# Kernel tuning notes

Measured on AMD Instinct MI355X. Metric: run time of the kernel, lower is better.

The kernel has to match this reference:

```python
import jax, jax.numpy as jnp
import numpy as np

EPSILON = 0.1


def setup_inputs() -> dict:
    key = jax.random.key(0)
    ks = jax.random.split(key, 6)
    N, E, F_IN, F_OUT, NF = 50000, 800000, 256, 96, 3
    x = jax.random.normal(ks[0], (N, F_IN), dtype=jnp.float32)
    adj_vals = jax.random.uniform(ks[1], (E,), dtype=jnp.float32)
    d_scales = jax.random.uniform(ks[2], (NF, N), dtype=jnp.float32)
    # xavier-uniform-ish weights
    limit = np.sqrt(6.0 / (F_IN + F_OUT)).astype(np.float32)
    weights = jax.random.uniform(ks[3], (NF, F_IN, F_OUT), dtype=jnp.float32,
                                 minval=-limit, maxval=limit)
    bias = jnp.zeros((F_OUT,), dtype=jnp.float32)
    edge_index = jax.random.randint(ks[4], (2, E), 0, N, dtype=jnp.int32)
    return {"x": x, "adj_vals": adj_vals, "d_scales": d_scales,
            "weights": weights, "bias": bias, "edge_index": edge_index}


def reference(x, adj_vals, d_scales, weights, bias, edge_index):
    N = x.shape[0]
    row, col = edge_index[0], edge_index[1]

    # degree with self loops (add_remaining_self_loops adds 1 per node)
    deg = jax.ops.segment_sum(jnp.ones_like(adj_vals), row, num_segments=N) + 1.0
    eps_deg_inv = EPSILON / deg  # [N], diagonal of sparse_degree(..., epsilon)

    def spmm(t):  # symadj @ t via edge list
        return jax.ops.segment_sum(adj_vals[:, None] * t[col], row, num_segments=N)

    out = jnp.zeros((N, weights.shape[2]), dtype=x.dtype)
    n_filters = weights.shape[0]
    for ii in range(n_filters):
        sign = -1.0 if ii == 0 else 1.0  # Ad = symadj -/+ eps*diag(deg^-1)
        t = d_scales[ii][:, None] * (x @ weights[ii])          # D @ (x W)
        t = spmm(t) + sign * eps_deg_inv[:, None] * t          # Ad @ t
        t = d_scales[ii][:, None] * jax.nn.relu(t)             # D @ relu(t)
        out = out + t
    return out + bias
```

## Files before the change

kernel.cpp:

```cpp
#include <hip/hip_runtime.h>

#define EPSILON 0.1f
#define F_IN 256
#define F_OUT 96
#define NF 3
#define TCOLS 288
#define TSTRIDE 320
#define CAP 64
#define BN 96
#define CW 104
#define NCVT (TCOLS * F_IN / 4)

#define RPB 64
#define NBINS 782
#define BCAP 1536
#define EPB 2048
#define GPAD 32

typedef __attribute__((ext_vector_type(8))) short bf8_t;
typedef __attribute__((ext_vector_type(4))) float f32x4;

__device__ inline ushort f2b(float f) {
    union { float f; unsigned u; } v; v.f = f;
    unsigned u = v.u;
    return (ushort)((u + 0x7FFFu + ((u >> 16) & 1u)) >> 16);
}
__device__ inline float blo(unsigned u) { return __uint_as_float(u << 16); }
__device__ inline float bhi(unsigned u) { return __uint_as_float(u & 0xffff0000u); }

__device__ inline bf8_t cvt8(float4 a, float4 b) {
    bf8_t r;
    r[0] = (short)f2b(a.x); r[1] = (short)f2b(a.y);
    r[2] = (short)f2b(a.z); r[3] = (short)f2b(a.w);
    r[4] = (short)f2b(b.x); r[5] = (short)f2b(b.y);
    r[6] = (short)f2b(b.z); r[7] = (short)f2b(b.w);
    return r;
}

__global__ __launch_bounds__(256) void setup_kernel(const float* __restrict__ w,
                                                    ushort* __restrict__ wt,
                                                    int* __restrict__ gcur) {
    int tid = blockIdx.x * 256 + threadIdx.x;
    if (tid < NCVT) {
        int base = tid * 4;
        int gc = base >> 8;
        int k  = base & 255;
        int ii = gc / F_OUT;
        int c  = gc - ii * F_OUT;
        const float* wp = w + (size_t)ii * (F_IN * F_OUT) + (size_t)k * F_OUT + c;
        ushort4 o;
        o.x = f2b(wp[0 * F_OUT]);
        o.y = f2b(wp[1 * F_OUT]);
        o.z = f2b(wp[2 * F_OUT]);
        o.w = f2b(wp[3 * F_OUT]);
        *(ushort4*)(wt + base) = o;
    } else {
        int z = (tid - NCVT) * 4;
        if (z + 3 < NBINS * GPAD) {
            *(int4*)(gcur + z) = make_int4(0, 0, 0, 0);
        }
    }
}

__global__ __launch_bounds__(256) void bin_cvt_kernel(
        const int* __restrict__ row, const int* __restrict__ col,
        const float* __restrict__ vals, int E,
        int* __restrict__ gcur, int2* __restrict__ gout,
        const float* __restrict__ x, ushort* __restrict__ xb, int N, int nbin) {
    __shared__ int hist[NBINS];
    __shared__ int gbase[NBINS];

    if ((int)blockIdx.x < nbin) {
        int tid = threadIdx.x;
        for (int i = tid; i < NBINS; i += 256) hist[i] = 0;
        __syncthreads();

        int e0 = (int)blockIdx.x * EPB;
        int4 r4[2], c4[2]; float4 v4[2];
        int rank[8], binv[8], valv[8];
        unsigned recx[8];
        #pragma unroll
        for (int g = 0; g < 2; ++g) {
            int e = e0 + tid * 4 + g * 1024;
            if (e + 3 < E) {
                r4[g] = *(const int4*)(row + e);
                c4[g] = *(const int4*)(col + e);
                v4[g] = *(const float4*)(vals + e);
            } else {
                int4 rr, cc; float4 vv;
                int* rp = (int*)&rr; int* cp = (int*)&cc; float* vp = (float*)&vv;
                #pragma unroll
                for (int j = 0; j < 4; ++j) {
                    int ee = e + j;
                    rp[j] = (ee < E) ? row[ee] : -1;
                    cp[j] = (ee < E) ? col[ee] : 0;
                    vp[j] = (ee < E) ? vals[ee] : 0.f;
                }
                r4[g] = rr; c4[g] = cc; v4[g] = vv;
            }
        }
        #pragma unroll
        for (int g = 0; g < 2; ++g) {
            const int* rp = (const int*)&r4[g];
            const int* cp = (const int*)&c4[g];
            const float* vp = (const float*)&v4[g];
            #pragma unroll
            for (int j = 0; j < 4; ++j) {
                int s = g * 4 + j;
                int r = rp[j];
                if (r >= 0) {
                    int b = r >> 6;
                    binv[s] = b;
                    recx[s] = (unsigned)(cp[j] & 0xffff) |
                              ((unsigned)(r & 63) << 16) | ((unsigned)b << 22);
                    valv[s] = __float_as_int(vp[j]);
                    rank[s] = atomicAdd(&hist[b], 1);
                } else {
                    binv[s] = -1; rank[s] = 0; recx[s] = 0; valv[s] = 0;
                }
            }
        }
        __syncthreads();

        #pragma unroll
        for (int q = 0; q < 4; ++q) {
            int i = threadIdx.x * 4 + q;
            if (i < NBINS) {
                int h = hist[i];
                gbase[i] = h ? atomicAdd(&gcur[i * GPAD], h) : 0;
            }
        }
        __syncthreads();

        #pragma unroll
        for (int s = 0; s < 8; ++s) {
            int b = binv[s];
            if (b >= 0) {
                int pos = gbase[b] + rank[s];
                if (pos < BCAP)
                    gout[(size_t)b * BCAP + pos] = make_int2((int)recx[s], valv[s]);
            }
        }
    } else {
        size_t base = ((size_t)((int)blockIdx.x - nbin) * 256 + threadIdx.x) * 8;
        if (base < (size_t)N * F_IN) {
            float4 a = *(const float4*)(x + base);
            float4 b = *(const float4*)(x + base + 4);
            bf8_t o = cvt8(a, b);
            *(bf8_t*)(xb + base) = o;
        }
    }
}

__global__ __launch_bounds__(512) void gemm_bucket(
        const ushort* __restrict__ xb, const ushort* __restrict__ wt,
        const float* __restrict__ dsc, ushort* __restrict__ t, int N,
        int nper, int nw,
        const int2* __restrict__ gout, const int* __restrict__ gcur,
        int* __restrict__ cnt, int2* __restrict__ evs2) {
    __shared__ ushort Bs[BN * F_IN];

    int tid = threadIdx.x;

    if ((int)blockIdx.x < NBINS) {
        int2* buck = (int2*)Bs;
        int*  lcnt = (int*)(Bs + 16384);
        int b = blockIdx.x;
        if (tid < RPB) lcnt[tid] = 0;
        __syncthreads();

        int nrec = gcur[b * GPAD];
        if (nrec > BCAP) nrec = BCAP;
        for (int i = tid; i < nrec; i += 512) {
            int2 rec = gout[(size_t)b * BCAP + i];
            int rl = (rec.x >> 16) & 63;
            int c  = rec.x & 0xffff;
            int k = atomicAdd(&lcnt[rl], 1);
            if (k < CAP) buck[rl * CAP + k] = make_int2(c * TSTRIDE, rec.y);
        }
        __syncthreads();

        int row0 = b * RPB;
        if (tid < RPB && row0 + tid < N) cnt[row0 + tid] = lcnt[tid];

        int lane = tid & 63, wave = tid >> 6;
        for (int r = wave; r < RPB; r += 8) {
            int rowg = row0 + r;
            if (rowg >= N) break;
            int m = min(lcnt[r], CAP);
            if (lane < m)
                evs2[(size_t)rowg * CAP + lane] = buck[r * CAP + lane];
        }
        return;
    }

    int lb = (int)blockIdx.x - NBINS;
    int xcd = lb & 7, li = lb >> 3;
    int w = xcd * nper + li;
    if (w >= nw) return;
    int mb = w / 3, cb = w - mb * 3;

    int lane = tid & 63, wave = tid >> 6;
    int cl = lane & 15, quad = lane >> 4;
    int gc0 = cb * BN;
    int m0 = mb * 128 + wave * 16;
    int mrow = m0 + cl;
    bool aok = (mrow < N);

    #pragma unroll
    for (int i = 0; i < 6; ++i) {
        int F = tid + i * 512;
        int rem = F & 63;
        int q = rem >> 4, c = rem & 15;
        int ksj = F >> 6;
        int ks = ksj / 6, j = ksj - ks * 6;
        int gc = gc0 + j * 16 + c;
        *(uint4*)(Bs + (size_t)F * 8) =
            *(const uint4*)(wt + (size_t)gc * F_IN + ks * 32 + q * 8);
    }

    uint4 areg[8];
    const ushort* xp = xb + (size_t)mrow * F_IN + quad * 8;
    const uint4 zu = make_uint4(0, 0, 0, 0);
    #pragma unroll
    for (int ks = 0; ks < 8; ++ks)
        areg[ks] = aok ? *(const uint4*)(xp + ks * 32) : zu;

    f32x4 acc[6];
    #pragma unroll
    for (int j = 0; j < 6; ++j) acc[j] = (f32x4){0.f, 0.f, 0.f, 0.f};

    __syncthreads();

    #pragma unroll
    for (int ks = 0; ks < 8; ++ks) {
        bf8_t a = *(const bf8_t*)&areg[ks];
        const ushort* bb = Bs + ((size_t)(ks * 6) * 64 + lane) * 8;
        #pragma unroll
        for (int j = 0; j < 6; ++j) {
            bf8_t b = *(const bf8_t*)(bb + j * 64 * 8);
            acc[j] = __builtin_amdgcn_mfma_f32_16x16x32_bf16(a, b, acc[j], 0, 0, 0);
        }
    }

    __syncthreads();
    ushort* Cw = Bs + wave * (16 * CW);
    float dscv[3][4];
    #pragma unroll
    for (int ii = 0; ii < 3; ++ii)
        #pragma unroll
        for (int r = 0; r < 4; ++r) {
            int rowg = m0 + quad * 4 + r;
            dscv[ii][r] = (rowg < N) ? dsc[(size_t)ii * N + rowg] : 0.f;
        }
    #pragma unroll
    for (int j = 0; j < 6; ++j) {
        int ii = (gc0 + j * 16) / F_OUT;
        #pragma unroll
        for (int r = 0; r < 4; ++r)
            Cw[(quad * 4 + r) * CW + j * 16 + cl] = f2b(dscv[ii][r] * acc[j][r]);
    }
    #pragma unroll
    for (int it = 0; it < 3; ++it) {
        int idx = lane + it * 64;
        int r = idx / 12, ch = idx - r * 12;
        int grow = m0 + r;
        if (grow < N)
            *(uint4*)(t + (size_t)grow * TSTRIDE + gc0 + ch * 8) =
                *(const uint4*)&Cw[r * CW + ch * 8];
    }
}

__device__ inline void acc8(float* acc, uint4 a, float v) {
    acc[0] = fmaf(v, blo(a.x), acc[0]); acc[1] = fmaf(v, bhi(a.x), acc[1]);
    acc[2] = fmaf(v, blo(a.y), acc[2]); acc[3] = fmaf(v, bhi(a.y), acc[3]);
    acc[4] = fmaf(v, blo(a.z), acc[4]); acc[5] = fmaf(v, bhi(a.z), acc[5]);
    acc[6] = fmaf(v, blo(a.w), acc[6]); acc[7] = fmaf(v, bhi(a.w), acc[7]);
}

__global__ __launch_bounds__(256) void spmm_kernel(const ushort* __restrict__ t,
                                                   const int2* __restrict__ evs2,
                                                   const int* __restrict__ cnt,
                                                   const float* __restrict__ dsc,
                                                   const float* __restrict__ bias,
                                                   float* __restrict__ out, int N) {
    int lane = threadIdx.x & 63;
    int wave = threadIdx.x >> 6;
    int n = blockIdx.x * 4 + wave;
    if (n >= N) return;

    int deg = cnt[n];
    int mm = (deg < CAP) ? deg : CAP;
    int s = n * CAP, e = s + mm;
    int coff = (lane < 40) ? lane * 8 : 0;

    float acc[8];
    #pragma unroll
    for (int j = 0; j < 8; ++j) acc[j] = 0.f;

    for (int base = s; base < e; base += 64) {
        int idx = base + lane;
        int2 q = make_int2(0, 0);
        if (idx < e) q = evs2[idx];
        int m = min(64, e - base);
        int j = 0;
        for (; j + 3 < m; j += 4) {
            int c0 = __shfl(q.x, j, 64);
            int c1 = __shfl(q.x, j + 1, 64);
            int c2 = __shfl(q.x, j + 2, 64);
            int c3 = __shfl(q.x, j + 3, 64);
            float v0 = __int_as_float(__shfl(q.y, j, 64));
            float v1 = __int_as_float(__shfl(q.y, j + 1, 64));
            float v2 = __int_as_float(__shfl(q.y, j + 2, 64));
            float v3 = __int_as_float(__shfl(q.y, j + 3, 64));
            uint4 a0 = *(const uint4*)(t + (size_t)c0 + coff);
            uint4 a1 = *(const uint4*)(t + (size_t)c1 + coff);
            uint4 a2 = *(const uint4*)(t + (size_t)c2 + coff);
            uint4 a3 = *(const uint4*)(t + (size_t)c3 + coff);
            acc8(acc, a0, v0);
            acc8(acc, a1, v1);
            acc8(acc, a2, v2);
            acc8(acc, a3, v3);
        }
        for (; j < m; ++j) {
            int c = __shfl(q.x, j, 64);
            float v = __int_as_float(__shfl(q.y, j, 64));
            uint4 a = *(const uint4*)(t + (size_t)c + coff);
            acc8(acc, a, v);
        }
    }

    float sign = (lane < 12) ? -1.f : 1.f;
    float epsdi = EPSILON / (float)(deg + 1);
    int ii = lane / 12;
    float dscv = (lane < 36) ? dsc[(size_t)ii * N + n] : 0.f;
    uint4 sv = *(const uint4*)(t + (size_t)n * TSTRIDE + coff);
    float se = sign * epsdi;
    float val[8];
    {
        unsigned u;
        u = sv.x; val[0] = fmaf(se, blo(u), acc[0]); val[1] = fmaf(se, bhi(u), acc[1]);
        u = sv.y; val[2] = fmaf(se, blo(u), acc[2]); val[3] = fmaf(se, bhi(u), acc[3]);
        u = sv.z; val[4] = fmaf(se, blo(u), acc[4]); val[5] = fmaf(se, bhi(u), acc[5]);
        u = sv.w; val[6] = fmaf(se, blo(u), acc[6]); val[7] = fmaf(se, bhi(u), acc[7]);
    }
    #pragma unroll
    for (int j = 0; j < 8; ++j) val[j] = fmaxf(val[j], 0.f) * dscv;

    float res[8];
    #pragma unroll
    for (int j = 0; j < 8; ++j) {
        float r1 = __shfl(val[j], lane + 12, 64);
        float r2 = __shfl(val[j], lane + 24, 64);
        res[j] = val[j] + r1 + r2;
    }
    if (lane < 12) {
        float4 b0 = *(const float4*)(bias + lane * 8);
        float4 b1 = *(const float4*)(bias + lane * 8 + 4);
        float4 o0 = make_float4(res[0] + b0.x, res[1] + b0.y, res[2] + b0.z, res[3] + b0.w);
        float4 o1 = make_float4(res[4] + b1.x, res[5] + b1.y, res[6] + b1.z, res[7] + b1.w);
        *(float4*)(out + (size_t)n * F_OUT + lane * 8) = o0;
        *(float4*)(out + (size_t)n * F_OUT + lane * 8 + 4) = o1;
    }
}

extern "C" void kernel_launch(void* const* d_in, const int* in_sizes, int n_in,
                              void* d_out, int out_size, void* d_ws, size_t ws_size,
                              hipStream_t stream) {
    const float* x    = (const float*)d_in[0];
    const float* adj  = (const float*)d_in[1];
    const float* dsc  = (const float*)d_in[2];
    const float* w    = (const float*)d_in[3];
    const float* bias = (const float*)d_in[4];
    const int*   ei   = (const int*)d_in[5];

    int E = in_sizes[1];
    int N = in_sizes[0] / F_IN;
    const int* row = ei;
    const int* col = ei + E;
    float* out = (float*)d_out;

    char* p = (char*)d_ws;
    auto take = [&](size_t bytes) {
        char* r = p;
        p += (bytes + 255) & ~(size_t)255;
        return r;
    };
    int*    cnt  = (int*)take((size_t)N * 4);
    int2*   evs2 = (int2*)take((size_t)N * CAP * 8);
    ushort* wt   = (ushort*)take((size_t)TCOLS * F_IN * 2);
    ushort* xb   = (ushort*)take((size_t)N * F_IN * 2);
    ushort* t    = (ushort*)take(((size_t)N * TSTRIDE + 256) * 2);
    int*    gcur = (int*)take((size_t)NBINS * GPAD * 4);
    int2*   gout = (int2*)take((size_t)NBINS * BCAP * 8);

    int nzero = (NBINS * GPAD + 3) / 4;
    setup_kernel<<<(NCVT + nzero + 255) / 256, 256, 0, stream>>>(w, wt, gcur);

    int nbin  = (E + EPB - 1) / EPB;
    int ncvtx = ((N * F_IN / 8) + 255) / 256;
    bin_cvt_kernel<<<nbin + ncvtx, 256, 0, stream>>>(row, col, adj, E, gcur, gout,
                                                     x, xb, N, nbin);

    int nt = (N + 127) / 128;
    int nw = 3 * nt;
    int nper = (((nw + 7) / 8) + 2) / 3 * 3;
    gemm_bucket<<<NBINS + 8 * nper, 512, 0, stream>>>(xb, wt, dsc, t, N, nper, nw,
                                                      gout, gcur, cnt, evs2);
    spmm_kernel<<<(N + 3) / 4, 256, 0, stream>>>(t, evs2, cnt, dsc, bias, out, N);
}
```

Baseline: 220.6 us.

## Fuse per-bin edge bucketing into SpMM kernel and drop evs2 round-trip

Moves the per-row edge bucketing out of the GEMM kernel and into the SpMM kernel, so each SpMM block builds its 64-row bucket list in shared memory and consumes it directly. This removes the global write and re-read of the evs2/cnt arrays. It also shrinks the t row stride from 320 to 288 and unrolls the gather loop by 8 with edge records read from LDS instead of wave shuffles. The cost is lower SpMM parallelism: 782 large blocks, each with a serial bucketing phase before any gather, plus more shared memory per block.

```diff
diff --git a/kernel.cpp b/kernel.cpp
--- a/kernel.cpp
+++ b/kernel.cpp
@@ -5,7 +5,7 @@
 #define F_OUT 96
 #define NF 3
 #define TCOLS 288
-#define TSTRIDE 320
+#define TSTRIDE 288
 #define CAP 64
 #define BN 96
 #define CW 104
@@ -152,49 +152,14 @@
     }
 }
 
-__global__ __launch_bounds__(512) void gemm_bucket(
+__global__ __launch_bounds__(512) void gemm_mfma(
         const ushort* __restrict__ xb, const ushort* __restrict__ wt,
         const float* __restrict__ dsc, ushort* __restrict__ t, int N,
-        int nper, int nw,
-        const int2* __restrict__ gout, const int* __restrict__ gcur,
-        int* __restrict__ cnt, int2* __restrict__ evs2) {
+        int nper, int nw) {
     __shared__ ushort Bs[BN * F_IN];
 
     int tid = threadIdx.x;
-
-    if ((int)blockIdx.x < NBINS) {
-        int2* buck = (int2*)Bs;
-        int*  lcnt = (int*)(Bs + 16384);
-        int b = blockIdx.x;
-        if (tid < RPB) lcnt[tid] = 0;
-        __syncthreads();
-
-        int nrec = gcur[b * GPAD];
-        if (nrec > BCAP) nrec = BCAP;
-        for (int i = tid; i < nrec; i += 512) {
-            int2 rec = gout[(size_t)b * BCAP + i];
-            int rl = (rec.x >> 16) & 63;
-            int c  = rec.x & 0xffff;
-            int k = atomicAdd(&lcnt[rl], 1);
-            if (k < CAP) buck[rl * CAP + k] = make_int2(c * TSTRIDE, rec.y);
-        }
-        __syncthreads();
-
-        int row0 = b * RPB;
-        if (tid < RPB && row0 + tid < N) cnt[row0 + tid] = lcnt[tid];
-
-        int lane = tid & 63, wave = tid >> 6;
-        for (int r = wave; r < RPB; r += 8) {
-            int rowg = row0 + r;
-            if (rowg >= N) break;
-            int m = min(lcnt[r], CAP);
-            if (lane < m)
-                evs2[(size_t)rowg * CAP + lane] = buck[r * CAP + lane];
-        }
-        return;
-    }
-
-    int lb = (int)blockIdx.x - NBINS;
+    int lb = (int)blockIdx.x;
     int xcd = lb & 7, li = lb >> 3;
     int w = xcd * nper + li;
     if (w >= nw) return;
@@ -278,89 +243,118 @@
     acc[6] = fmaf(v, blo(a.w), acc[6]); acc[7] = fmaf(v, bhi(a.w), acc[7]);
 }
 
-__global__ __launch_bounds__(256) void spmm_kernel(const ushort* __restrict__ t,
-                                                   const int2* __restrict__ evs2,
-                                                   const int* __restrict__ cnt,
-                                                   const float* __restrict__ dsc,
-                                                   const float* __restrict__ bias,
-                                                   float* __restrict__ out, int N) {
-    int lane = threadIdx.x & 63;
-    int wave = threadIdx.x >> 6;
-    int n = blockIdx.x * 4 + wave;
-    if (n >= N) return;
-
-    int deg = cnt[n];
-    int mm = (deg < CAP) ? deg : CAP;
-    int s = n * CAP, e = s + mm;
-    int coff = (lane < 40) ? lane * 8 : 0;
-
-    float acc[8];
-    #pragma unroll
-    for (int j = 0; j < 8; ++j) acc[j] = 0.f;
-
-    for (int base = s; base < e; base += 64) {
-        int idx = base + lane;
-        int2 q = make_int2(0, 0);
-        if (idx < e) q = evs2[idx];
-        int m = min(64, e - base);
+__global__ __launch_bounds__(512) void spmm_kernel(
+        const ushort* __restrict__ t,
+        const int2* __restrict__ gout, const int* __restrict__ gcur,
+        const float* __restrict__ dsc, const float* __restrict__ bias,
+        float* __restrict__ out, int N) {
+    __shared__ int2 buck[RPB * CAP];
+    __shared__ int lcnt[RPB];
+
+    int tid = threadIdx.x;
+    int b = blockIdx.x;
+    if (tid < RPB) lcnt[tid] = 0;
+    __syncthreads();
+
+    int nrec = gcur[b * GPAD];
+    if (nrec > BCAP) nrec = BCAP;
+    for (int i = tid; i < nrec; i += 512) {
+        int2 rec = gout[(size_t)b * BCAP + i];
+        int rl = (rec.x >> 16) & 63;
+        int c  = rec.x & 0xffff;
+        int k = atomicAdd(&lcnt[rl], 1);
+        if (k < CAP) buck[rl * CAP + k] = make_int2(c * TSTRIDE, rec.y);
+    }
+    __syncthreads();
+
+    int lane = tid & 63, wave = tid >> 6;
+    int row0 = b * RPB;
+    int coff = (lane < 36) ? lane * 8 : 0;
+
+    for (int rr = wave; rr < RPB; rr += 8) {
+        int n = row0 + rr;
+        if (n >= N) break;
+        int deg = lcnt[rr];
+        int m = (deg < CAP) ? deg : CAP;
+        const int2* bp = buck + rr * CAP;
+
+        uint4 sv = *(const uint4*)(t + (size_t)n * TSTRIDE + coff);
+
+        float acc[8];
+        #pragma unroll
+        for (int j = 0; j < 8; ++j) acc[j] = 0.f;
+
         int j = 0;
+        for (; j + 7 < m; j += 8) {
+            int2 q0 = bp[j],     q1 = bp[j + 1], q2 = bp[j + 2], q3 = bp[j + 3];
+            int2 q4 = bp[j + 4], q5 = bp[j + 5], q6 = bp[j + 6], q7 = bp[j + 7];
+            uint4 a0 = *(const uint4*)(t + (size_t)q0.x + coff);
+            uint4 a1 = *(const uint4*)(t + (size_t)q1.x + coff);
+            uint4 a2 = *(const uint4*)(t + (size_t)q2.x + coff);
+            uint4 a3 = *(const uint4*)(t + (size_t)q3.x + coff);
+            uint4 a4 = *(const uint4*)(t + (size_t)q4.x + coff);
+            uint4 a5 = *(const uint4*)(t + (size_t)q5.x + coff);
+            uint4 a6 = *(const uint4*)(t + (size_t)q6.x + coff);
+            uint4 a7 = *(const uint4*)(t + (size_t)q7.x + coff);
+            acc8(acc, a0, __int_as_float(q0.y));
+            acc8(acc, a1, __int_as_float(q1.y));
+            acc8(acc, a2, __int_as_float(q2.y));
+            acc8(acc, a3, __int_as_float(q3.y));
+            acc8(acc, a4, __int_as_float(q4.y));
+            acc8(acc, a5, __int_as_float(q5.y));
+            acc8(acc, a6, __int_as_float(q6.y));
+            acc8(acc, a7, __int_as_float(q7.y));
+        }
         for (; j + 3 < m; j += 4) {
-            int c0 = __shfl(q.x, j, 64);
-            int c1 = __shfl(q.x, j + 1, 64);
-            int c2 = __shfl(q.x, j + 2, 64);
-            int c3 = __shfl(q.x, j + 3, 64);
-            float v0 = __int_as_float(__shfl(q.y, j, 64));
-            float v1 = __int_as_float(__shfl(q.y, j + 1, 64));
-            float v2 = __int_as_float(__shfl(q.y, j + 2, 64));
-            float v3 = __int_as_float(__shfl(q.y, j + 3, 64));
-            uint4 a0 = *(const uint4*)(t + (size_t)c0 + coff);
-            uint4 a1 = *(const uint4*)(t + (size_t)c1 + coff);
-            uint4 a2 = *(const uint4*)(t + (size_t)c2 + coff);
-            uint4 a3 = *(const uint4*)(t + (size_t)c3 + coff);
-            acc8(acc, a0, v0);
-            acc8(acc, a1, v1);
-            acc8(acc, a2, v2);
-            acc8(acc, a3, v3);
+            int2 q0 = bp[j], q1 = bp[j + 1], q2 = bp[j + 2], q3 = bp[j + 3];
+            uint4 a0 = *(const uint4*)(t + (size_t)q0.x + coff);
+            uint4 a1 = *(const uint4*)(t + (size_t)q1.x + coff);
+            uint4 a2 = *(const uint4*)(t + (size_t)q2.x + coff);
+            uint4 a3 = *(const uint4*)(t + (size_t)q3.x + coff);
+            acc8(acc, a0, __int_as_float(q0.y));
+            acc8(acc, a1, __int_as_float(q1.y));
+            acc8(acc, a2, __int_as_float(q2.y));
+            acc8(acc, a3, __int_as_float(q3.y));
         }
         for (; j < m; ++j) {
-            int c = __shfl(q.x, j, 64);
-            float v = __int_as_float(__shfl(q.y, j, 64));
-            uint4 a = *(const uint4*)(t + (size_t)c + coff);
-            acc8(acc, a, v);
-        }
-    }
-
-    float sign = (lane < 12) ? -1.f : 1.f;
-    float epsdi = EPSILON / (float)(deg + 1);
-    int ii = lane / 12;
-    float dscv = (lane < 36) ? dsc[(size_t)ii * N + n] : 0.f;
-    uint4 sv = *(const uint4*)(t + (size_t)n * TSTRIDE + coff);
-    float se = sign * epsdi;
-    float val[8];
-    {
-        unsigned u;
-        u = sv.x; val[0] = fmaf(se, blo(u), acc[0]); val[1] = fmaf(se, bhi(u), acc[1]);
-        u = sv.y; val[2] = fmaf(se, blo(u), acc[2]); val[3] = fmaf(se, bhi(u), acc[3]);
-        u = sv.z; val[4] = fmaf(se, blo(u), acc[4]); val[5] = fmaf(se, bhi(u), acc[5]);
-        u = sv.w; val[6] = fmaf(se, blo(u), acc[6]); val[7] = fmaf(se, bhi(u), acc[7]);
-    }
-    #pragma unroll
-    for (int j = 0; j < 8; ++j) val[j] = fmaxf(val[j], 0.f) * dscv;
-
-    float res[8];
-    #pragma unroll
-    for (int j = 0; j < 8; ++j) {
-        float r1 = __shfl(val[j], lane + 12, 64);
-        float r2 = __shfl(val[j], lane + 24, 64);
-        res[j] = val[j] + r1 + r2;
-    }
-    if (lane < 12) {
-        float4 b0 = *(const float4*)(bias + lane * 8);
-        float4 b1 = *(const float4*)(bias + lane * 8 + 4);
-        float4 o0 = make_float4(res[0] + b0.x, res[1] + b0.y, res[2] + b0.z, res[3] + b0.w);
-        float4 o1 = make_float4(res[4] + b1.x, res[5] + b1.y, res[6] + b1.z, res[7] + b1.w);
-        *(float4*)(out + (size_t)n * F_OUT + lane * 8) = o0;
-        *(float4*)(out + (size_t)n * F_OUT + lane * 8 + 4) = o1;
+            int2 q = bp[j];
+            uint4 a = *(const uint4*)(t + (size_t)q.x + coff);
+            acc8(acc, a, __int_as_float(q.y));
+        }
+
+        float sign = (lane < 12) ? -1.f : 1.f;
+        float epsdi = EPSILON / (float)(deg + 1);
+        int ii = lane / 12;
+        float dscv = (lane < 36) ? dsc[(size_t)ii * N + n] : 0.f;
+        float se = sign * epsdi;
+        float val[8];
+        {
+            unsigned u;
+            u = sv.x; val[0] = fmaf(se, blo(u), acc[0]); val[1] = fmaf(se, bhi(u), acc[1]);
+            u = sv.y; val[2] = fmaf(se, blo(u), acc[2]); val[3] = fmaf(se, bhi(u), acc[3]);
+            u = sv.z; val[4] = fmaf(se, blo(u), acc[4]); val[5] = fmaf(se, bhi(u), acc[5]);
+            u = sv.w; val[6] = fmaf(se, blo(u), acc[6]); val[7] = fmaf(se, bhi(u), acc[7]);
+        }
+        #pragma unroll
+        for (int j2 = 0; j2 < 8; ++j2) val[j2] = fmaxf(val[j2], 0.f) * dscv;
+
+        float res[8];
+        #pragma unroll
+        for (int j2 = 0; j2 < 8; ++j2) {
+            float r1 = __shfl(val[j2], lane + 12, 64);
+            float r2 = __shfl(val[j2], lane + 24, 64);
+            res[j2] = val[j2] + r1 + r2;
+        }
+        if (lane < 12) {
+            float4 b0 = *(const float4*)(bias + lane * 8);
+            float4 b1 = *(const float4*)(bias + lane * 8 + 4);
+            float4 o0 = make_float4(res[0] + b0.x, res[1] + b0.y,
+                                    res[2] + b0.z, res[3] + b0.w);
+            float4 o1 = make_float4(res[4] + b1.x, res[5] + b1.y,
+                                    res[6] + b1.z, res[7] + b1.w);
+            *(float4*)(out + (size_t)n * F_OUT + lane * 8) = o0;
+            *(float4*)(out + (size_t)n * F_OUT + lane * 8 + 4) = o1;
+        }
     }
 }
 
@@ -386,8 +380,6 @@
         p += (bytes + 255) & ~(size_t)255;
         return r;
     };
-    int*    cnt  = (int*)take((size_t)N * 4);
-    int2*   evs2 = (int2*)take((size_t)N * CAP * 8);
     ushort* wt   = (ushort*)take((size_t)TCOLS * F_IN * 2);
     ushort* xb   = (ushort*)take((size_t)N * F_IN * 2);
     ushort* t    = (ushort*)take(((size_t)N * TSTRIDE + 256) * 2);
@@ -405,7 +397,7 @@
     int nt = (N + 127) / 128;
     int nw = 3 * nt;
     int nper = (((nw + 7) / 8) + 2) / 3 * 3;
-    gemm_bucket<<<NBINS + 8 * nper, 512, 0, stream>>>(xb, wt, dsc, t, N, nper, nw,
-                                                      gout, gcur, cnt, evs2);
-    spmm_kernel<<<(N + 3) / 4, 256, 0, stream>>>(t, evs2, cnt, dsc, bias, out, N);
-}
+    gemm_mfma<<<8 * nper, 512, 0, stream>>>(xb, wt, dsc, t, N, nper, nw);
+
+    spmm_kernel<<<NBINS, 512, 0, stream>>>(t, gout, gcur, dsc, bias, out, N);
+}
```

Measured after the change: 221.7 us. About the same (+0.5%).

## Split intermediate into 8 column planes for cache-friendly SpMM gathers

Applied to the files above, without the earlier changes.

The bf16 intermediate t is stored as 8 separate planes of 36 columns (72 bytes per row) instead of one 320-element padded row. The SpMM kernel assigns each block a plane and a 64-row chunk, with 7 edges processed in parallel per wave (9 lanes each), and reduces across lanes with shuffles. Each plane is small enough to improve L2/MALL locality for the random column gathers and drops the padding traffic. The cost is more shuffle reductions, narrower 8-byte loads, and repeated edge-list reads across the 8 planes. The bucket LDS stride is also padded to 65 to reduce bank conflicts.

```diff
diff --git a/kernel.cpp b/kernel.cpp
--- a/kernel.cpp
+++ b/kernel.cpp
@@ -5,7 +5,6 @@
 #define F_OUT 96
 #define NF 3
 #define TCOLS 288
-#define TSTRIDE 320
 #define CAP 64
 #define BN 96
 #define CW 104
@@ -16,6 +15,7 @@
 #define BCAP 1536
 #define EPB 2048
 #define GPAD 32
+
 
 typedef __attribute__((ext_vector_type(8))) short bf8_t;
 typedef __attribute__((ext_vector_type(4))) float f32x4;
@@ -155,7 +155,7 @@
 __global__ __launch_bounds__(512) void gemm_bucket(
         const ushort* __restrict__ xb, const ushort* __restrict__ wt,
         const float* __restrict__ dsc, ushort* __restrict__ t, int N,
-        int nper, int nw,
+        int nper, int nw, int plnu,
         const int2* __restrict__ gout, const int* __restrict__ gcur,
         int* __restrict__ cnt, int2* __restrict__ evs2) {
     __shared__ ushort Bs[BN * F_IN];
@@ -164,7 +164,7 @@
 
     if ((int)blockIdx.x < NBINS) {
         int2* buck = (int2*)Bs;
-        int*  lcnt = (int*)(Bs + 16384);
+        int*  lcnt = (int*)(Bs + 16640);
         int b = blockIdx.x;
         if (tid < RPB) lcnt[tid] = 0;
         __syncthreads();
@@ -176,7 +176,7 @@
             int rl = (rec.x >> 16) & 63;
             int c  = rec.x & 0xffff;
             int k = atomicAdd(&lcnt[rl], 1);
-            if (k < CAP) buck[rl * CAP + k] = make_int2(c * TSTRIDE, rec.y);
+            if (k < CAP) buck[rl * 65 + k] = make_int2(c * 72, rec.y);
         }
         __syncthreads();
 
@@ -189,7 +189,7 @@
             if (rowg >= N) break;
             int m = min(lcnt[r], CAP);
             if (lane < m)
-                evs2[(size_t)rowg * CAP + lane] = buck[r * CAP + lane];
+                evs2[(size_t)rowg * CAP + lane] = buck[r * 65 + lane];
         }
         return;
     }
@@ -245,122 +245,101 @@
 
     __syncthreads();
     ushort* Cw = Bs + wave * (16 * CW);
-    float dscv[3][4];
-    #pragma unroll
-    for (int ii = 0; ii < 3; ++ii)
-        #pragma unroll
-        for (int r = 0; r < 4; ++r) {
-            int rowg = m0 + quad * 4 + r;
-            dscv[ii][r] = (rowg < N) ? dsc[(size_t)ii * N + rowg] : 0.f;
-        }
+    float dscr[4];
+    #pragma unroll
+    for (int r = 0; r < 4; ++r) {
+        int rowg = m0 + quad * 4 + r;
+        dscr[r] = (rowg < N) ? dsc[(size_t)cb * N + rowg] : 0.f;
+    }
     #pragma unroll
     for (int j = 0; j < 6; ++j) {
-        int ii = (gc0 + j * 16) / F_OUT;
         #pragma unroll
         for (int r = 0; r < 4; ++r)
-            Cw[(quad * 4 + r) * CW + j * 16 + cl] = f2b(dscv[ii][r] * acc[j][r]);
-    }
-    #pragma unroll
-    for (int it = 0; it < 3; ++it) {
-        int idx = lane + it * 64;
-        int r = idx / 12, ch = idx - r * 12;
+            Cw[(quad * 4 + r) * CW + j * 16 + cl] = f2b(dscr[r] * acc[j][r]);
+    }
+    #pragma unroll
+    for (int it = 0; it < 6; ++it) {
+        int idx = it * 64 + lane;
+        int r = idx / 24, c = idx - r * 24;
         int grow = m0 + r;
+        int pl = c / 3, cl3 = c - pl * 3;
         if (grow < N)
-            *(uint4*)(t + (size_t)grow * TSTRIDE + gc0 + ch * 8) =
-                *(const uint4*)&Cw[r * CW + ch * 8];
-    }
-}
-
-__device__ inline void acc8(float* acc, uint4 a, float v) {
-    acc[0] = fmaf(v, blo(a.x), acc[0]); acc[1] = fmaf(v, bhi(a.x), acc[1]);
-    acc[2] = fmaf(v, blo(a.y), acc[2]); acc[3] = fmaf(v, bhi(a.y), acc[3]);
-    acc[4] = fmaf(v, blo(a.z), acc[4]); acc[5] = fmaf(v, bhi(a.z), acc[5]);
-    acc[6] = fmaf(v, blo(a.w), acc[6]); acc[7] = fmaf(v, bhi(a.w), acc[7]);
-}
-
-__global__ __launch_bounds__(256) void spmm_kernel(const ushort* __restrict__ t,
-                                                   const int2* __restrict__ evs2,
-                                                   const int* __restrict__ cnt,
-                                                   const float* __restrict__ dsc,
-                                                   const float* __restrict__ bias,
-                                                   float* __restrict__ out, int N) {
-    int lane = threadIdx.x & 63;
-    int wave = threadIdx.x >> 6;
-    int n = blockIdx.x * 4 + wave;
-    if (n >= N) return;
-
-    int deg = cnt[n];
-    int mm = (deg < CAP) ? deg : CAP;
-    int s = n * CAP, e = s + mm;
-    int coff = (lane < 40) ? lane * 8 : 0;
-
-    float acc[8];
-    #pragma unroll
-    for (int j = 0; j < 8; ++j) acc[j] = 0.f;
-
-    for (int base = s; base < e; base += 64) {
-        int idx = base + lane;
-        int2 q = make_int2(0, 0);
-        if (idx < e) q = evs2[idx];
-        int m = min(64, e - base);
-        int j = 0;
-        for (; j + 3 < m; j += 4) {
-            int c0 = __shfl(q.x, j, 64);
-            int c1 = __shfl(q.x, j + 1, 64);
-            int c2 = __shfl(q.x, j + 2, 64);
-            int c3 = __shfl(q.x, j + 3, 64);
-            float v0 = __int_as_float(__shfl(q.y, j, 64));
-            float v1 = __int_as_float(__shfl(q.y, j + 1, 64));
-            float v2 = __int_as_float(__shfl(q.y, j + 2, 64));
-            float v3 = __int_as_float(__shfl(q.y, j + 3, 64));
-            uint4 a0 = *(const uint4*)(t + (size_t)c0 + coff);
-            uint4 a1 = *(const uint4*)(t + (size_t)c1 + coff);
-            uint4 a2 = *(const uint4*)(t + (size_t)c2 + coff);
-            uint4 a3 = *(const uint4*)(t + (size_t)c3 + coff);
-            acc8(acc, a0, v0);
-            acc8(acc, a1, v1);
-            acc8(acc, a2, v2);
-            acc8(acc, a3, v3);
-        }
-        for (; j < m; ++j) {
-            int c = __shfl(q.x, j, 64);
-            float v = __int_as_float(__shfl(q.y, j, 64));
-            uint4 a = *(const uint4*)(t + (size_t)c + coff);
-            acc8(acc, a, v);
-        }
-    }
-
-    float sign = (lane < 12) ? -1.f : 1.f;
-    float epsdi = EPSILON / (float)(deg + 1);
-    int ii = lane / 12;
-    float dscv = (lane < 36) ? dsc[(size_t)ii * N + n] : 0.f;
-    uint4 sv = *(const uint4*)(t + (size_t)n * TSTRIDE + coff);
-    float se = sign * epsdi;
-    float val[8];
-    {
-        unsigned u;
-        u = sv.x; val[0] = fmaf(se, blo(u), acc[0]); val[1] = fmaf(se, bhi(u), acc[1]);
-        u = sv.y; val[2] = fmaf(se, blo(u), acc[2]); val[3] = fmaf(se, bhi(u), acc[3]);
-        u = sv.z; val[4] = fmaf(se, blo(u), acc[4]); val[5] = fmaf(se, bhi(u), acc[5]);
-        u = sv.w; val[6] = fmaf(se, blo(u), acc[6]); val[7] = fmaf(se, bhi(u), acc[7]);
-    }
-    #pragma unroll
-    for (int j = 0; j < 8; ++j) val[j] = fmaxf(val[j], 0.f) * dscv;
-
-    float res[8];
-    #pragma unroll
-    for (int j = 0; j < 8; ++j) {
-        float r1 = __shfl(val[j], lane + 12, 64);
-        float r2 = __shfl(val[j], lane + 24, 64);
-        res[j] = val[j] + r1 + r2;
-    }
-    if (lane < 12) {
-        float4 b0 = *(const float4*)(bias + lane * 8);
-        float4 b1 = *(const float4*)(bias + lane * 8 + 4);
-        float4 o0 = make_float4(res[0] + b0.x, res[1] + b0.y, res[2] + b0.z, res[3] + b0.w);
-        float4 o1 = make_float4(res[4] + b1.x, res[5] + b1.y, res[6] + b1.z, res[7] + b1.w);
-        *(float4*)(out + (size_t)n * F_OUT + lane * 8) = o0;
-        *(float4*)(out + (size_t)n * F_OUT + lane * 8 + 4) = o1;
+            *(uint2*)(t + (size_t)pl * plnu + (size_t)grow * 36 + cb * 12 + cl3 * 4) =
+                *(const uint2*)&Cw[r * CW + c * 4];
+    }
+}
+
+__global__ __launch_bounds__(512) void spmm_kernel(
+        const ushort* __restrict__ t, const int2* __restrict__ evs2,
+        const int* __restrict__ cnt, const float* __restrict__ dsc,
+        const float* __restrict__ bias, float* __restrict__ out,
+        int N, int plnu) {
+    int tid = threadIdx.x;
+    int lane = tid & 63, wave = tid >> 6;
+    int g = blockIdx.x;
+    int p = g & 7;
+    int row0 = (g >> 3) * 64;
+    const char* pb = (const char*)(t + (size_t)p * (size_t)plnu);
+    int e = lane / 9;
+    int q = lane - e * 9;
+    const char* pbq = pb + q * 8;
+
+    for (int rr = wave; rr < 64; rr += 8) {
+        int n = row0 + rr;
+        if (n >= N) break;
+        int deg = cnt[n];
+        int mm = (deg < CAP) ? deg : CAP;
+        int2 rec = make_int2(0, 0);
+        if (lane < mm) rec = evs2[(size_t)n * CAP + lane];
+        uint2 sv = *(const uint2*)(pb + (size_t)n * 72 + q * 8);
+
+        float a0 = 0.f, a1 = 0.f, a2 = 0.f, a3 = 0.f;
+        for (int o = 0; o < mm; o += 14) {
+            int eg0 = o + e, eg1 = o + 7 + e;
+            int   co0 = __shfl(rec.x, eg0 & 63, 64);
+            float v0  = __int_as_float(__shfl(rec.y, eg0 & 63, 64));
+            int   co1 = __shfl(rec.x, eg1 & 63, 64);
+            float v1  = __int_as_float(__shfl(rec.y, eg1 & 63, 64));
+            v0 = (e < 7 && eg0 < mm) ? v0 : 0.f;
+            v1 = (e < 7 && eg1 < mm) ? v1 : 0.f;
+            uint2 A = *(const uint2*)(pbq + co0);
+            uint2 B = *(const uint2*)(pbq + co1);
+            a0 = fmaf(v0, blo(A.x), a0); a1 = fmaf(v0, bhi(A.x), a1);
+            a2 = fmaf(v0, blo(A.y), a2); a3 = fmaf(v0, bhi(A.y), a3);
+            a0 = fmaf(v1, blo(B.x), a0); a1 = fmaf(v1, bhi(B.x), a1);
+            a2 = fmaf(v1, blo(B.y), a2); a3 = fmaf(v1, bhi(B.y), a3);
+        }
+
+        #pragma unroll
+        for (int off = 36; off >= 9; off >>= 1) {
+            int s = lane + off; s = (s > 63) ? 63 : s;
+            a0 += __shfl(a0, s, 64);
+            a1 += __shfl(a1, s, 64);
+            a2 += __shfl(a2, s, 64);
+            a3 += __shfl(a3, s, 64);
+        }
+
+        float sign = (q < 3) ? -1.f : 1.f;
+        float se = sign * (EPSILON / (float)(deg + 1));
+        float dscv = dsc[(size_t)(q / 3) * N + n];
+        float v0 = fmaf(se, blo(sv.x), a0);
+        float v1 = fmaf(se, bhi(sv.x), a1);
+        float v2 = fmaf(se, blo(sv.y), a2);
+        float v3 = fmaf(se, bhi(sv.y), a3);
+        v0 = fmaxf(v0, 0.f) * dscv; v1 = fmaxf(v1, 0.f) * dscv;
+        v2 = fmaxf(v2, 0.f) * dscv; v3 = fmaxf(v3, 0.f) * dscv;
+
+        int s3 = lane + 3; s3 = (s3 > 63) ? 63 : s3;
+        int s6 = lane + 6; s6 = (s6 > 63) ? 63 : s6;
+        float r0 = v0 + __shfl(v0, s3, 64) + __shfl(v0, s6, 64);
+        float r1 = v1 + __shfl(v1, s3, 64) + __shfl(v1, s6, 64);
+        float r2 = v2 + __shfl(v2, s3, 64) + __shfl(v2, s6, 64);
+        float r3 = v3 + __shfl(v3, s3, 64) + __shfl(v3, s6, 64);
+        if (lane < 3) {
+            float4 bb = *(const float4*)(bias + p * 12 + lane * 4);
+            float4 o4 = make_float4(r0 + bb.x, r1 + bb.y, r2 + bb.z, r3 + bb.w);
+            *(float4*)(out + (size_t)n * F_OUT + p * 12 + lane * 4) = o4;
+        }
     }
 }
 
@@ -379,6 +358,8 @@
     const int* row = ei;
     const int* col = ei + E;
     float* out = (float*)d_out;
+
+    int plnu = (int)(((size_t)N * 36 + 127) & ~(size_t)127);
 
     char* p = (char*)d_ws;
     auto take = [&](size_t bytes) {
@@ -390,7 +371,7 @@
     int2*   evs2 = (int2*)take((size_t)N * CAP * 8);
     ushort* wt   = (ushort*)take((size_t)TCOLS * F_IN * 2);
     ushort* xb   = (ushort*)take((size_t)N * F_IN * 2);
-    ushort* t    = (ushort*)take(((size_t)N * TSTRIDE + 256) * 2);
+    ushort* t    = (ushort*)take((size_t)8 * plnu * 2 + 256);
     int*    gcur = (int*)take((size_t)NBINS * GPAD * 4);
     int2*   gout = (int2*)take((size_t)NBINS * BCAP * 8);
 
@@ -406,6 +387,8 @@
     int nw = 3 * nt;
     int nper = (((nw + 7) / 8) + 2) / 3 * 3;
     gemm_bucket<<<NBINS + 8 * nper, 512, 0, stream>>>(xb, wt, dsc, t, N, nper, nw,
-                                                      gout, gcur, cnt, evs2);
-    spmm_kernel<<<(N + 3) / 4, 256, 0, stream>>>(t, evs2, cnt, dsc, bias, out, N);
-}
+                                                      plnu, gout, gcur, cnt, evs2);
+
+    int nchunk = (N + 63) / 64;
+    spmm_kernel<<<8 * nchunk, 512, 0, stream>>>(t, evs2, cnt, dsc, bias, out, N, plnu);
+}
```

Result: slower. 285.7 us (+29.5%).
